# Kernel tuning notes

Measured on AMD Instinct MI355X. Metric: run time of the kernel, lower is better.

Reference implementation:

```python
import jax, jax.numpy as jnp
import numpy as np

B_SZ, L, N, H = 8, 4096, 256, 256
R_MIN, R_MAX, MAX_PHASE = 0.0, 1.0, 0.314


def setup_inputs() -> dict:
    key = jax.random.key(0)
    ks = jax.random.split(key, 8)
    x = jax.random.normal(ks[0], (B_SZ, L, H), jnp.float32)
    def glorot(k, shape):
        return jax.random.normal(k, shape, jnp.float32) * jnp.sqrt(2.0 / (shape[0] + shape[1])).astype(jnp.float32)
    B_re = glorot(ks[1], (N, H))
    B_im = glorot(ks[2], (N, H))
    C_re = glorot(ks[3], (H, N))
    C_im = glorot(ks[4], (H, N))
    # DiskRingRadius / DiskRingPhase initializers
    u1 = jax.random.uniform(ks[5], (N,), jnp.float32, 1e-6, 1.0)
    u2 = jax.random.uniform(ks[6], (N,), jnp.float32, 1e-6, 1.0)
    nu_log = jnp.log(-0.5 * jnp.log(u1 * (R_MAX ** 2 - R_MIN ** 2) + R_MIN ** 2))
    theta_log = jnp.log(MAX_PHASE * u2)
    D = jax.random.normal(ks[7], (H,), jnp.float32) * 0.05  # RandomNormal(stddev=0.05)
    return dict(x=x, B_re=B_re, B_im=B_im, C_re=C_re, C_im=C_im,
                nu_log=nu_log, theta_log=theta_log, D=D)


def reference(x, B_re, B_im, C_re, C_im, nu_log, theta_log, D):
    # Diagonal complex recurrence parameters
    Lambda = jnp.exp(jax.lax.complex(-jnp.exp(nu_log), jnp.exp(theta_log)))  # [N]
    gamma = jnp.sqrt(1.0 - jnp.abs(Lambda) ** 2).astype(jnp.complex64)       # [N]
    B_norm = (B_re + 1j * B_im).astype(jnp.complex64) * gamma[:, None]       # [N,H]
    C = (C_re + 1j * C_im).astype(jnp.complex64)                             # [H,N]

    # Input projection: [B,L,N] complex
    Bu = jnp.einsum('blh,nh->bln', x.astype(jnp.complex64), B_norm)
    Lambda_el = jnp.broadcast_to(Lambda, Bu.shape)

    def combine(a, b):
        la, ba = a
        lb, bb = b
        return (la * lb, lb * ba + bb)

    _, states = jax.lax.associative_scan(combine, (Lambda_el, Bu), axis=1)  # [B,L,N]

    y = jnp.real(jnp.einsum('bln,hn->blh', states, C))
    y = y + x * D  # H_in == H -> elementwise skip
    return y
```

## Files before the change

kernel.cpp:

```cpp
#include <hip/hip_runtime.h>
#include <hip/hip_bf16.h>
#include <math.h>

#define B_SZ 8
#define LSEQ 4096
#define NDIM 256
#define HDIM 256
#define MROWS (B_SZ * LSEQ)
#define CH 64
#define NC (LSEQ / CH)

#define BM 64
#define BN 128
#define BK 32
#define PAD 40
#define SSTR 68

typedef _Float16 half8 __attribute__((ext_vector_type(8)));
typedef _Float16 half4 __attribute__((ext_vector_type(4)));
typedef float fx4 __attribute__((ext_vector_type(4)));

__global__ void k_prep(const float* __restrict__ Bre, const float* __restrict__ Bim,
                       const float* __restrict__ Cre, const float* __restrict__ Cim,
                       const float* __restrict__ nu_log, const float* __restrict__ th_log,
                       _Float16* __restrict__ BreH, _Float16* __restrict__ BimH,
                       _Float16* __restrict__ CreH, _Float16* __restrict__ CimNH,
                       float* __restrict__ lamRe, float* __restrict__ lamIm,
                       float* __restrict__ powRe, float* __restrict__ powIm) {
    int r = blockIdx.x;
    int t = threadIdx.x;
    float nu  = expf(nu_log[r]);
    float th  = expf(th_log[r]);
    float mod = expf(-nu);
    float g   = sqrtf(fmaxf(1.0f - mod * mod, 0.0f));
    if (t == 0) {
        lamRe[r] = mod * cosf(th);
        lamIm[r] = mod * sinf(th);
    }
    int i = r * 256 + t;
    BreH[i]  = (_Float16)(Bre[i] * g);
    BimH[i]  = (_Float16)(Bim[i] * g);
    CreH[i]  = (_Float16)Cre[i];
    CimNH[i] = (_Float16)(-Cim[i]);
    if (r < CH) {
        float nuN = expf(nu_log[t]);
        float thN = expf(th_log[t]);
        float k   = (float)(r + 1);
        float mo  = expf(-nuN * k);
        powRe[r * 256 + t] = mo * cosf(thN * k);
        powIm[r * 256 + t] = mo * sinf(thN * k);
    }
}

__launch_bounds__(256)
__global__ void k_buscan(const float* __restrict__ x,
                         const _Float16* __restrict__ BreH,
                         const _Float16* __restrict__ BimH,
                         const float* __restrict__ lamRe,
                         const float* __restrict__ lamIm,
                         _Float16* __restrict__ stReH,
                         _Float16* __restrict__ stImH,
                         float* __restrict__ finRe,
                         float* __restrict__ finIm) {
    __shared__ __align__(16) _Float16 smem[25600];

    const int tid  = threadIdx.x;
    const int lane = tid & 63;
    const int wave = tid >> 6;
    const int wr   = wave >> 1;
    const int wc   = wave & 1;
    const int m0   = blockIdx.x * BM;
    const int n0   = blockIdx.y * BN;

    const int ar = tid >> 2, ac = (tid & 3) * 8;
    const int br = tid >> 1, bc = (tid & 1) * 16;

    const int fRC = lane & 15;
    const int fKg = (lane >> 4) * 8;

    fx4 accR[8], accI[8];
#pragma unroll
    for (int i = 0; i < 8; ++i) { accR[i] = (fx4)0.0f; accI[i] = (fx4)0.0f; }

    float4 xf0, xf1;
    half8 w0, w1, w2, w3;

    {
        const float* xp = x + (size_t)(m0 + ar) * HDIM + ac;
        xf0 = *(const float4*)xp;
        xf1 = *(const float4*)(xp + 4);
        const _Float16* bp1 = BreH + (size_t)(n0 + br) * HDIM + bc;
        const _Float16* bp2 = BimH + (size_t)(n0 + br) * HDIM + bc;
        w0 = *(const half8*)bp1;  w1 = *(const half8*)(bp1 + 8);
        w2 = *(const half8*)bp2;  w3 = *(const half8*)(bp2 + 8);
        half8 hv;
        hv[0]=(_Float16)xf0.x; hv[1]=(_Float16)xf0.y; hv[2]=(_Float16)xf0.z; hv[3]=(_Float16)xf0.w;
        hv[4]=(_Float16)xf1.x; hv[5]=(_Float16)xf1.y; hv[6]=(_Float16)xf1.z; hv[7]=(_Float16)xf1.w;
        *(half8*)&smem[ar * PAD + ac] = hv;
        *(half8*)&smem[2560 + br * PAD + bc] = w0;  *(half8*)&smem[2560 + br * PAD + bc + 8] = w1;
        *(half8*)&smem[7680 + br * PAD + bc] = w2;  *(half8*)&smem[7680 + br * PAD + bc + 8] = w3;
    }
    __syncthreads();

    int p = 0;
    for (int k0 = 0; k0 < HDIM; k0 += BK) {
        const int po = p * 12800;
        const bool nx = (k0 + BK) < HDIM;
        if (nx) {
            const float* xp = x + (size_t)(m0 + ar) * HDIM + k0 + BK + ac;
            xf0 = *(const float4*)xp;
            xf1 = *(const float4*)(xp + 4);
            const _Float16* bp1 = BreH + (size_t)(n0 + br) * HDIM + k0 + BK + bc;
            const _Float16* bp2 = BimH + (size_t)(n0 + br) * HDIM + k0 + BK + bc;
            w0 = *(const half8*)bp1;  w1 = *(const half8*)(bp1 + 8);
            w2 = *(const half8*)bp2;  w3 = *(const half8*)(bp2 + 8);
        }
        half8 af[2], bRf[4], bIf[4];
#pragma unroll
        for (int sm = 0; sm < 2; ++sm)
            af[sm] = *(const half8*)&smem[po + (wr * 32 + sm * 16 + fRC) * PAD + fKg];
#pragma unroll
        for (int sn = 0; sn < 4; ++sn) {
            bRf[sn] = *(const half8*)&smem[po + 2560 + (wc * 64 + sn * 16 + fRC) * PAD + fKg];
            bIf[sn] = *(const half8*)&smem[po + 7680 + (wc * 64 + sn * 16 + fRC) * PAD + fKg];
        }
#pragma unroll
        for (int sm = 0; sm < 2; ++sm)
#pragma unroll
            for (int sn = 0; sn < 4; ++sn) {
                accR[sm * 4 + sn] = __builtin_amdgcn_mfma_f32_16x16x32_f16(af[sm], bRf[sn], accR[sm * 4 + sn], 0, 0, 0);
                accI[sm * 4 + sn] = __builtin_amdgcn_mfma_f32_16x16x32_f16(af[sm], bIf[sn], accI[sm * 4 + sn], 0, 0, 0);
            }
        if (nx) {
            const int qo = (p ^ 1) * 12800;
            half8 hv;
            hv[0]=(_Float16)xf0.x; hv[1]=(_Float16)xf0.y; hv[2]=(_Float16)xf0.z; hv[3]=(_Float16)xf0.w;
            hv[4]=(_Float16)xf1.x; hv[5]=(_Float16)xf1.y; hv[6]=(_Float16)xf1.z; hv[7]=(_Float16)xf1.w;
            *(half8*)&smem[qo + ar * PAD + ac] = hv;
            *(half8*)&smem[qo + 2560 + br * PAD + bc] = w0;  *(half8*)&smem[qo + 2560 + br * PAD + bc + 8] = w1;
            *(half8*)&smem[qo + 7680 + br * PAD + bc] = w2;  *(half8*)&smem[qo + 7680 + br * PAD + bc + 8] = w3;
        }
        __syncthreads();
        p ^= 1;
    }

    _Float16* SRe = smem;
    _Float16* SIm = smem + 8704;

    const int rBase = (lane >> 4) * 4;
#pragma unroll
    for (int sm = 0; sm < 2; ++sm)
#pragma unroll
        for (int sn = 0; sn < 4; ++sn) {
            int col = wc * 64 + sn * 16 + fRC;
            int row = wr * 32 + sm * 16 + rBase;
            half4 h1, h2;
#pragma unroll
            for (int reg = 0; reg < 4; ++reg) {
                h1[reg] = (_Float16)accR[sm * 4 + sn][reg];
                h2[reg] = (_Float16)accI[sm * 4 + sn][reg];
            }
            *(half4*)&SRe[col * SSTR + row] = h1;
            *(half4*)&SIm[col * SSTR + row] = h2;
        }
    __syncthreads();

    if (tid < BN) {
        int col = tid;
        int n = n0 + col;
        float lr = lamRe[n], li = lamIm[n];
        _Float16* cR = &SRe[col * SSTR];
        _Float16* cI = &SIm[col * SSTR];
        float sr = 0.0f, si = 0.0f;
#pragma unroll 8
        for (int r = 0; r < CH; ++r) {
            float ur = (float)cR[r];
            float ui = (float)cI[r];
            float nr = fmaf(lr, sr, fmaf(-li, si, ur));
            float ni = fmaf(lr, si, fmaf(li, sr, ui));
            sr = nr; si = ni;
            cR[r] = (_Float16)sr;
            cI[r] = (_Float16)si;
        }
        int bb = blockIdx.x >> 6, cc = blockIdx.x & 63;
        size_t f = ((size_t)(bb * NC + cc)) * NDIM + n;
        finRe[f] = sr;
        finIm[f] = si;
    }
    __syncthreads();

    {
        int row = tid >> 2;
        int cb  = (tid & 3) * 32;
        size_t gbase = (size_t)(m0 + row) * NDIM + n0 + cb;
#pragma unroll
        for (int g = 0; g < 4; ++g) {
            half8 h1, h2;
#pragma unroll
            for (int e = 0; e < 8; ++e) {
                int col = cb + g * 8 + e;
                h1[e] = SRe[col * SSTR + row];
                h2[e] = SIm[col * SSTR + row];
            }
            *(half8*)(stReH + gbase + g * 8) = h1;
            *(half8*)(stImH + gbase + g * 8) = h2;
        }
    }
}

__launch_bounds__(256)
__global__ void k_carry(const float* __restrict__ lamRe,
                        const float* __restrict__ lamIm,
                        const float* __restrict__ finRe,
                        const float* __restrict__ finIm,
                        float* __restrict__ carRe,
                        float* __restrict__ carIm) {
    const int b = blockIdx.x;
    const int n = threadIdx.x;
    const float lr = lamRe[n];
    const float li = lamIm[n];
    float kr = 1.0f, ki = 0.0f;
#pragma unroll
    for (int i = 0; i < CH; ++i) {
        float t = kr * lr - ki * li;
        ki = fmaf(kr, li, ki * lr);
        kr = t;
    }
    float cr = 0.0f, ci = 0.0f;
#pragma unroll 8
    for (int c = 0; c < NC; ++c) {
        size_t idx = ((size_t)b * NC + c) * NDIM + n;
        carRe[idx] = cr;
        carIm[idx] = ci;
        float fr = finRe[idx];
        float fi = finIm[idx];
        float t = fmaf(kr, cr, fmaf(-ki, ci, fr));
        ci = fmaf(kr, ci, fmaf(ki, cr, fi));
        cr = t;
    }
}

__launch_bounds__(256)
__global__ void k_out(const _Float16* __restrict__ sReH,
                      const _Float16* __restrict__ sImH,
                      const _Float16* __restrict__ CreH,
                      const _Float16* __restrict__ CimNH,
                      const float* __restrict__ powRe,
                      const float* __restrict__ powIm,
                      const float* __restrict__ carRe,
                      const float* __restrict__ carIm,
                      const float* __restrict__ x,
                      const float* __restrict__ Dv,
                      float* __restrict__ y) {
    __shared__ __align__(16) _Float16 A1[2][BM * PAD];
    __shared__ __align__(16) _Float16 A2[2][BM * PAD];
    __shared__ __align__(16) _Float16 Cr[2][BN * PAD];
    __shared__ __align__(16) _Float16 Ci[2][BN * PAD];

    const int tid  = threadIdx.x;
    const int lane = tid & 63;
    const int wave = tid >> 6;
    const int wr   = wave >> 1;
    const int wc   = wave & 1;
    const int m0   = blockIdx.x * BM;
    const int h0   = blockIdx.y * BN;
    const int chunk = m0 >> 6;

    const int ar = tid >> 2, ac = (tid & 3) * 8;
    const int br = tid >> 1, bc = (tid & 1) * 16;

    const int fRC = lane & 15;
    const int fKg = (lane >> 4) * 8;

    fx4 acc[8];
#pragma unroll
    for (int i = 0; i < 8; ++i) acc[i] = (fx4)0.0f;

    half8 s1, s2, c0a, c0b, c1a, c1b;
    float4 pr0, pr1, pi0, pi1, cr0, cr1, ci0, ci1;

#define LOAD_STAGE(K0)                                                          \
    {                                                                           \
        size_t aOff = (size_t)(m0 + ar) * NDIM + (K0) + ac;                     \
        s1 = *(const half8*)(sReH + aOff);                                      \
        s2 = *(const half8*)(sImH + aOff);                                      \
        size_t pOff = (size_t)ar * NDIM + (K0) + ac;                            \
        pr0 = *(const float4*)(powRe + pOff); pr1 = *(const float4*)(powRe + pOff + 4); \
        pi0 = *(const float4*)(powIm + pOff); pi1 = *(const float4*)(powIm + pOff + 4); \
        size_t cOff = (size_t)chunk * NDIM + (K0) + ac;                         \
        cr0 = *(const float4*)(carRe + cOff); cr1 = *(const float4*)(carRe + cOff + 4); \
        ci0 = *(const float4*)(carIm + cOff); ci1 = *(const float4*)(carIm + cOff + 4); \
        const _Float16* cp1 = CreH  + (size_t)(h0 + br) * NDIM + (K0) + bc;     \
        const _Float16* cp2 = CimNH + (size_t)(h0 + br) * NDIM + (K0) + bc;     \
        c0a = *(const half8*)cp1;  c0b = *(const half8*)(cp1 + 8);              \
        c1a = *(const half8*)cp2;  c1b = *(const half8*)(cp2 + 8);              \
    }

#define WRITE_STAGE(P)                                                          \
    {                                                                           \
        float prA[8] = {pr0.x,pr0.y,pr0.z,pr0.w,pr1.x,pr1.y,pr1.z,pr1.w};       \
        float piA[8] = {pi0.x,pi0.y,pi0.z,pi0.w,pi1.x,pi1.y,pi1.z,pi1.w};       \
        float crA[8] = {cr0.x,cr0.y,cr0.z,cr0.w,cr1.x,cr1.y,cr1.z,cr1.w};       \
        float ciA[8] = {ci0.x,ci0.y,ci0.z,ci0.w,ci1.x,ci1.y,ci1.z,ci1.w};       \
        half8 h1, h2;                                                           \
        _Pragma("unroll")                                                       \
        for (int e = 0; e < 8; ++e) {                                           \
            float ur = fmaf(prA[e], crA[e], fmaf(-piA[e], ciA[e], (float)s1[e])); \
            float ui = fmaf(prA[e], ciA[e], fmaf( piA[e], crA[e], (float)s2[e])); \
            h1[e] = (_Float16)ur; h2[e] = (_Float16)ui;                         \
        }                                                                       \
        *(half8*)&A1[P][ar * PAD + ac] = h1;                                    \
        *(half8*)&A2[P][ar * PAD + ac] = h2;                                    \
        *(half8*)&Cr[P][br * PAD + bc] = c0a;  *(half8*)&Cr[P][br * PAD + bc + 8] = c0b; \
        *(half8*)&Ci[P][br * PAD + bc] = c1a;  *(half8*)&Ci[P][br * PAD + bc + 8] = c1b; \
    }

    LOAD_STAGE(0);
    WRITE_STAGE(0);
    __syncthreads();

    int p = 0;
    for (int k0 = 0; k0 < NDIM; k0 += BK) {
        const bool nx = (k0 + BK) < NDIM;
        if (nx) LOAD_STAGE(k0 + BK);
        half8 a1[2], a2[2], bRf[4], bIf[4];
#pragma unroll
        for (int sm = 0; sm < 2; ++sm) {
            a1[sm] = *(const half8*)&A1[p][(wr * 32 + sm * 16 + fRC) * PAD + fKg];
            a2[sm] = *(const half8*)&A2[p][(wr * 32 + sm * 16 + fRC) * PAD + fKg];
        }
#pragma unroll
        for (int sn = 0; sn < 4; ++sn) {
            bRf[sn] = *(const half8*)&Cr[p][(wc * 64 + sn * 16 + fRC) * PAD + fKg];
            bIf[sn] = *(const half8*)&Ci[p][(wc * 64 + sn * 16 + fRC) * PAD + fKg];
        }
#pragma unroll
        for (int sm = 0; sm < 2; ++sm)
#pragma unroll
            for (int sn = 0; sn < 4; ++sn) {
                acc[sm * 4 + sn] = __builtin_amdgcn_mfma_f32_16x16x32_f16(a1[sm], bRf[sn], acc[sm * 4 + sn], 0, 0, 0);
                acc[sm * 4 + sn] = __builtin_amdgcn_mfma_f32_16x16x32_f16(a2[sm], bIf[sn], acc[sm * 4 + sn], 0, 0, 0);
            }
        if (nx) WRITE_STAGE(p ^ 1);
        __syncthreads();
        p ^= 1;
    }

    float d[4];
#pragma unroll
    for (int sn = 0; sn < 4; ++sn) d[sn] = Dv[h0 + wc * 64 + sn * 16 + fRC];

    const int rBase = (lane >> 4) * 4;
#pragma unroll
    for (int sm = 0; sm < 2; ++sm)
#pragma unroll
        for (int sn = 0; sn < 4; ++sn) {
            int h = h0 + wc * 64 + sn * 16 + fRC;
#pragma unroll
            for (int reg = 0; reg < 4; ++reg) {
                int m = m0 + wr * 32 + sm * 16 + rBase + reg;
                size_t idx = (size_t)m * HDIM + h;
                y[idx] = fmaf(x[idx], d[sn], acc[sm * 4 + sn][reg]);
            }
        }
#undef LOAD_STAGE
#undef WRITE_STAGE
}

extern "C" void kernel_launch(void* const* d_in, const int* in_sizes, int n_in,
                              void* d_out, int out_size, void* d_ws, size_t ws_size,
                              hipStream_t stream) {
    const float* x      = (const float*)d_in[0];
    const float* B_re   = (const float*)d_in[1];
    const float* B_im   = (const float*)d_in[2];
    const float* C_re   = (const float*)d_in[3];
    const float* C_im   = (const float*)d_in[4];
    const float* nu_log = (const float*)d_in[5];
    const float* th_log = (const float*)d_in[6];
    const float* D      = (const float*)d_in[7];
    float* y = (float*)d_out;

    char* p = (char*)d_ws;
    _Float16* stReH = (_Float16*)p;  p += (size_t)MROWS * NDIM * 2;
    _Float16* stImH = (_Float16*)p;  p += (size_t)MROWS * NDIM * 2;
    _Float16* BreH  = (_Float16*)p;  p += (size_t)NDIM * HDIM * 2;
    _Float16* BimH  = (_Float16*)p;  p += (size_t)NDIM * HDIM * 2;
    _Float16* CreH  = (_Float16*)p;  p += (size_t)HDIM * NDIM * 2;
    _Float16* CimNH = (_Float16*)p;  p += (size_t)HDIM * NDIM * 2;
    float* lamRe = (float*)p;  p += NDIM * 4;
    float* lamIm = (float*)p;  p += NDIM * 4;
    float* powRe = (float*)p;  p += (size_t)CH * NDIM * 4;
    float* powIm = (float*)p;  p += (size_t)CH * NDIM * 4;
    float* finRe = (float*)p;  p += (size_t)B_SZ * NC * NDIM * 4;
    float* finIm = (float*)p;  p += (size_t)B_SZ * NC * NDIM * 4;
    float* carRe = (float*)p;  p += (size_t)B_SZ * NC * NDIM * 4;
    float* carIm = (float*)p;  p += (size_t)B_SZ * NC * NDIM * 4;

    k_prep<<<NDIM, 256, 0, stream>>>(B_re, B_im, C_re, C_im, nu_log, th_log,
                                     BreH, BimH, CreH, CimNH, lamRe, lamIm,
                                     powRe, powIm);

    dim3 gGemm(MROWS / BM, NDIM / BN);
    k_buscan<<<gGemm, 256, 0, stream>>>(x, BreH, BimH, lamRe, lamIm,
                                        stReH, stImH, finRe, finIm);

    k_carry<<<B_SZ, 256, 0, stream>>>(lamRe, lamIm, finRe, finIm, carRe, carIm);

    dim3 gOut(MROWS / BM, HDIM / BN);
    k_out<<<gOut, 256, 0, stream>>>(stReH, stImH, CreH, CimNH,
                                    powRe, powIm, carRe, carIm, x, D, y);
}
```

Measured before the change: 162.0 us.

## Swizzle LDS tiles, parallelize carry scan with wave shuffles, coalesce state stores

Replaces padded LDS tiles with an unpadded XOR-swizzled layout in both GEMM kernels, cutting LDS footprint and avoiding bank conflicts on fragment reads. The MFMA loops now load B fragments in two phases (real then imaginary) to lower register pressure. The cross-chunk carry kernel changes from a serial loop over 64 chunks per thread (8 blocks) to a per-wave Kogge-Stone complex scan using shuffles over 2048 waves. The state store pattern is reshuffled so that adjacent threads write adjacent 16-byte segments.

Result: faster. 150.9 us, median of 3 (-6.8%).

```diff
diff --git a/kernel.cpp b/kernel.cpp
--- a/kernel.cpp
+++ b/kernel.cpp
@@ -13,7 +13,6 @@
 #define BM 64
 #define BN 128
 #define BK 32
-#define PAD 40
 #define SSTR 68
 
 typedef _Float16 half8 __attribute__((ext_vector_type(8)));
@@ -62,7 +61,7 @@
                          _Float16* __restrict__ stImH,
                          float* __restrict__ finRe,
                          float* __restrict__ finIm) {
-    __shared__ __align__(16) _Float16 smem[25600];
+    __shared__ __align__(16) _Float16 smem[20480];
 
     const int tid  = threadIdx.x;
     const int lane = tid & 63;
@@ -73,10 +72,15 @@
     const int n0   = blockIdx.y * BN;
 
     const int ar = tid >> 2, ac = (tid & 3) * 8;
-    const int br = tid >> 1, bc = (tid & 1) * 16;
-
-    const int fRC = lane & 15;
-    const int fKg = (lane >> 4) * 8;
+    const int aw = ar * 32 + (((tid & 3) ^ ((tid >> 3) & 3)) * 8);
+
+    const int br = tid >> 1, g2 = tid & 1, bc = g2 * 16;
+    const int fb = (br >> 1) & 3;
+    const int bw0 = br * 32 + (((2 * g2)     ^ fb) * 8);
+    const int bw1 = br * 32 + (((2 * g2 + 1) ^ fb) * 8);
+
+    const int fRC   = lane & 15;
+    const int rslot = (((lane >> 4) ^ (fRC >> 1)) & 3) * 8;
 
     fx4 accR[8], accI[8];
 #pragma unroll
@@ -85,64 +89,64 @@
     float4 xf0, xf1;
     half8 w0, w1, w2, w3;
 
-    {
-        const float* xp = x + (size_t)(m0 + ar) * HDIM + ac;
-        xf0 = *(const float4*)xp;
-        xf1 = *(const float4*)(xp + 4);
-        const _Float16* bp1 = BreH + (size_t)(n0 + br) * HDIM + bc;
-        const _Float16* bp2 = BimH + (size_t)(n0 + br) * HDIM + bc;
-        w0 = *(const half8*)bp1;  w1 = *(const half8*)(bp1 + 8);
-        w2 = *(const half8*)bp2;  w3 = *(const half8*)(bp2 + 8);
-        half8 hv;
-        hv[0]=(_Float16)xf0.x; hv[1]=(_Float16)xf0.y; hv[2]=(_Float16)xf0.z; hv[3]=(_Float16)xf0.w;
-        hv[4]=(_Float16)xf1.x; hv[5]=(_Float16)xf1.y; hv[6]=(_Float16)xf1.z; hv[7]=(_Float16)xf1.w;
-        *(half8*)&smem[ar * PAD + ac] = hv;
-        *(half8*)&smem[2560 + br * PAD + bc] = w0;  *(half8*)&smem[2560 + br * PAD + bc + 8] = w1;
-        *(half8*)&smem[7680 + br * PAD + bc] = w2;  *(half8*)&smem[7680 + br * PAD + bc + 8] = w3;
-    }
+#define LOAD_T(K0)                                                          \
+    {                                                                       \
+        const float* xp = x + (size_t)(m0 + ar) * HDIM + (K0) + ac;         \
+        xf0 = *(const float4*)xp;                                           \
+        xf1 = *(const float4*)(xp + 4);                                     \
+        const _Float16* bp1 = BreH + (size_t)(n0 + br) * HDIM + (K0) + bc;  \
+        const _Float16* bp2 = BimH + (size_t)(n0 + br) * HDIM + (K0) + bc;  \
+        w0 = *(const half8*)bp1;  w1 = *(const half8*)(bp1 + 8);            \
+        w2 = *(const half8*)bp2;  w3 = *(const half8*)(bp2 + 8);            \
+    }
+#define WRITE_T(PO)                                                         \
+    {                                                                       \
+        half8 hv;                                                           \
+        hv[0]=(_Float16)xf0.x; hv[1]=(_Float16)xf0.y; hv[2]=(_Float16)xf0.z; hv[3]=(_Float16)xf0.w; \
+        hv[4]=(_Float16)xf1.x; hv[5]=(_Float16)xf1.y; hv[6]=(_Float16)xf1.z; hv[7]=(_Float16)xf1.w; \
+        *(half8*)&smem[(PO) + aw] = hv;                                     \
+        *(half8*)&smem[(PO) + 2048 + bw0] = w0;                             \
+        *(half8*)&smem[(PO) + 2048 + bw1] = w1;                             \
+        *(half8*)&smem[(PO) + 6144 + bw0] = w2;                             \
+        *(half8*)&smem[(PO) + 6144 + bw1] = w3;                             \
+    }
+
+    LOAD_T(0);
+    WRITE_T(0);
     __syncthreads();
 
     int p = 0;
     for (int k0 = 0; k0 < HDIM; k0 += BK) {
-        const int po = p * 12800;
+        const int po = p * 10240;
+        const int qo = (p ^ 1) * 10240;
         const bool nx = (k0 + BK) < HDIM;
-        if (nx) {
-            const float* xp = x + (size_t)(m0 + ar) * HDIM + k0 + BK + ac;
-            xf0 = *(const float4*)xp;
-            xf1 = *(const float4*)(xp + 4);
-            const _Float16* bp1 = BreH + (size_t)(n0 + br) * HDIM + k0 + BK + bc;
-            const _Float16* bp2 = BimH + (size_t)(n0 + br) * HDIM + k0 + BK + bc;
-            w0 = *(const half8*)bp1;  w1 = *(const half8*)(bp1 + 8);
-            w2 = *(const half8*)bp2;  w3 = *(const half8*)(bp2 + 8);
-        }
-        half8 af[2], bRf[4], bIf[4];
-#pragma unroll
-        for (int sm = 0; sm < 2; ++sm)
-            af[sm] = *(const half8*)&smem[po + (wr * 32 + sm * 16 + fRC) * PAD + fKg];
-#pragma unroll
-        for (int sn = 0; sn < 4; ++sn) {
-            bRf[sn] = *(const half8*)&smem[po + 2560 + (wc * 64 + sn * 16 + fRC) * PAD + fKg];
-            bIf[sn] = *(const half8*)&smem[po + 7680 + (wc * 64 + sn * 16 + fRC) * PAD + fKg];
-        }
-#pragma unroll
-        for (int sm = 0; sm < 2; ++sm)
-#pragma unroll
-            for (int sn = 0; sn < 4; ++sn) {
-                accR[sm * 4 + sn] = __builtin_amdgcn_mfma_f32_16x16x32_f16(af[sm], bRf[sn], accR[sm * 4 + sn], 0, 0, 0);
-                accI[sm * 4 + sn] = __builtin_amdgcn_mfma_f32_16x16x32_f16(af[sm], bIf[sn], accI[sm * 4 + sn], 0, 0, 0);
-            }
-        if (nx) {
-            const int qo = (p ^ 1) * 12800;
-            half8 hv;
-            hv[0]=(_Float16)xf0.x; hv[1]=(_Float16)xf0.y; hv[2]=(_Float16)xf0.z; hv[3]=(_Float16)xf0.w;
-            hv[4]=(_Float16)xf1.x; hv[5]=(_Float16)xf1.y; hv[6]=(_Float16)xf1.z; hv[7]=(_Float16)xf1.w;
-            *(half8*)&smem[qo + ar * PAD + ac] = hv;
-            *(half8*)&smem[qo + 2560 + br * PAD + bc] = w0;  *(half8*)&smem[qo + 2560 + br * PAD + bc + 8] = w1;
-            *(half8*)&smem[qo + 7680 + br * PAD + bc] = w2;  *(half8*)&smem[qo + 7680 + br * PAD + bc + 8] = w3;
-        }
+        if (nx) LOAD_T(k0 + BK);
+        half8 af[2], bf[4];
+#pragma unroll
+        for (int sm = 0; sm < 2; ++sm)
+            af[sm] = *(const half8*)&smem[po + (wr * 32 + sm * 16 + fRC) * 32 + rslot];
+#pragma unroll
+        for (int sn = 0; sn < 4; ++sn)
+            bf[sn] = *(const half8*)&smem[po + 2048 + (wc * 64 + sn * 16 + fRC) * 32 + rslot];
+#pragma unroll
+        for (int sm = 0; sm < 2; ++sm)
+#pragma unroll
+            for (int sn = 0; sn < 4; ++sn)
+                accR[sm * 4 + sn] = __builtin_amdgcn_mfma_f32_16x16x32_f16(af[sm], bf[sn], accR[sm * 4 + sn], 0, 0, 0);
+#pragma unroll
+        for (int sn = 0; sn < 4; ++sn)
+            bf[sn] = *(const half8*)&smem[po + 6144 + (wc * 64 + sn * 16 + fRC) * 32 + rslot];
+#pragma unroll
+        for (int sm = 0; sm < 2; ++sm)
+#pragma unroll
+            for (int sn = 0; sn < 4; ++sn)
+                accI[sm * 4 + sn] = __builtin_amdgcn_mfma_f32_16x16x32_f16(af[sm], bf[sn], accI[sm * 4 + sn], 0, 0, 0);
+        if (nx) WRITE_T(qo);
         __syncthreads();
         p ^= 1;
     }
+#undef LOAD_T
+#undef WRITE_T
 
     _Float16* SRe = smem;
     _Float16* SIm = smem + 8704;
@@ -191,19 +195,19 @@
 
     {
         int row = tid >> 2;
-        int cb  = (tid & 3) * 32;
+        int cb  = (tid & 3) * 8;
         size_t gbase = (size_t)(m0 + row) * NDIM + n0 + cb;
 #pragma unroll
         for (int g = 0; g < 4; ++g) {
             half8 h1, h2;
 #pragma unroll
             for (int e = 0; e < 8; ++e) {
-                int col = cb + g * 8 + e;
+                int col = cb + g * 32 + e;
                 h1[e] = SRe[col * SSTR + row];
                 h2[e] = SIm[col * SSTR + row];
             }
-            *(half8*)(stReH + gbase + g * 8) = h1;
-            *(half8*)(stImH + gbase + g * 8) = h2;
+            *(half8*)(stReH + gbase + g * 32) = h1;
+            *(half8*)(stImH + gbase + g * 32) = h2;
         }
     }
 }
@@ -215,29 +219,46 @@
                         const float* __restrict__ finIm,
                         float* __restrict__ carRe,
                         float* __restrict__ carIm) {
-    const int b = blockIdx.x;
-    const int n = threadIdx.x;
-    const float lr = lamRe[n];
-    const float li = lamIm[n];
-    float kr = 1.0f, ki = 0.0f;
-#pragma unroll
-    for (int i = 0; i < CH; ++i) {
-        float t = kr * lr - ki * li;
-        ki = fmaf(kr, li, ki * lr);
-        kr = t;
-    }
-    float cr = 0.0f, ci = 0.0f;
-#pragma unroll 8
-    for (int c = 0; c < NC; ++c) {
-        size_t idx = ((size_t)b * NC + c) * NDIM + n;
-        carRe[idx] = cr;
-        carIm[idx] = ci;
-        float fr = finRe[idx];
-        float fi = finIm[idx];
-        float t = fmaf(kr, cr, fmaf(-ki, ci, fr));
-        ci = fmaf(kr, ci, fmaf(ki, cr, fi));
-        cr = t;
-    }
+    const int tid  = threadIdx.x;
+    const int lane = tid & 63;
+    const int wv   = tid >> 6;
+    const int idx  = blockIdx.x * 4 + wv;
+    const int b    = idx >> 8;
+    const int n    = idx & 255;
+
+    float plr = lamRe[n], pli = lamIm[n];
+#pragma unroll
+    for (int i = 0; i < 6; ++i) {
+        float t = plr * plr - pli * pli;
+        pli = 2.0f * plr * pli;
+        plr = t;
+    }
+
+    size_t base = ((size_t)(b * NC + lane)) * NDIM + n;
+    float vr = finRe[base];
+    float vi = finIm[base];
+
+#pragma unroll
+    for (int d = 1; d < 64; d <<= 1) {
+        float vpr = __shfl_up(vr, d);
+        float vpi = __shfl_up(vi, d);
+        float lpr = __shfl_up(plr, d);
+        float lpi = __shfl_up(pli, d);
+        if (lane >= d) {
+            float nvr = fmaf(plr, vpr, fmaf(-pli, vpi, vr));
+            float nvi = fmaf(plr, vpi, fmaf(pli, vpr, vi));
+            vr = nvr; vi = nvi;
+            float t = plr * lpr - pli * lpi;
+            pli = fmaf(plr, lpi, pli * lpr);
+            plr = t;
+        }
+    }
+
+    float cr = __shfl_up(vr, 1);
+    float ci = __shfl_up(vi, 1);
+    if (lane == 0) { cr = 0.0f; ci = 0.0f; }
+    carRe[base] = cr;
+    carIm[base] = ci;
 }
 
 __launch_bounds__(256)
@@ -252,10 +273,10 @@
                       const float* __restrict__ x,
                       const float* __restrict__ Dv,
                       float* __restrict__ y) {
-    __shared__ __align__(16) _Float16 A1[2][BM * PAD];
-    __shared__ __align__(16) _Float16 A2[2][BM * PAD];
-    __shared__ __align__(16) _Float16 Cr[2][BN * PAD];
-    __shared__ __align__(16) _Float16 Ci[2][BN * PAD];
+    __shared__ __align__(16) _Float16 sA1[2][2048];
+    __shared__ __align__(16) _Float16 sA2[2][2048];
+    __shared__ __align__(16) _Float16 sCr[2][4096];
+    __shared__ __align__(16) _Float16 sCi[2][4096];
 
     const int tid  = threadIdx.x;
     const int lane = tid & 63;
@@ -267,10 +288,15 @@
     const int chunk = m0 >> 6;
 
     const int ar = tid >> 2, ac = (tid & 3) * 8;
-    const int br = tid >> 1, bc = (tid & 1) * 16;
-
-    const int fRC = lane & 15;
-    const int fKg = (lane >> 4) * 8;
+    const int aw = ar * 32 + (((tid & 3) ^ ((tid >> 3) & 3)) * 8);
+
+    const int br = tid >> 1, g2 = tid & 1, bc = g2 * 16;
+    const int fb = (br >> 1) & 3;
+    const int bw0 = br * 32 + (((2 * g2)     ^ fb) * 8);
+    const int bw1 = br * 32 + (((2 * g2 + 1) ^ fb) * 8);
+
+    const int fRC   = lane & 15;
+    const int rslot = (((lane >> 4) ^ (fRC >> 1)) & 3) * 8;
 
     fx4 acc[8];
 #pragma unroll
@@ -279,72 +305,78 @@
     half8 s1, s2, c0a, c0b, c1a, c1b;
     float4 pr0, pr1, pi0, pi1, cr0, cr1, ci0, ci1;
 
-#define LOAD_STAGE(K0)                                                          \
-    {                                                                           \
-        size_t aOff = (size_t)(m0 + ar) * NDIM + (K0) + ac;                     \
-        s1 = *(const half8*)(sReH + aOff);                                      \
-        s2 = *(const half8*)(sImH + aOff);                                      \
-        size_t pOff = (size_t)ar * NDIM + (K0) + ac;                            \
+#define LOAD_T(K0)                                                          \
+    {                                                                       \
+        size_t aOff = (size_t)(m0 + ar) * NDIM + (K0) + ac;                 \
+        s1 = *(const half8*)(sReH + aOff);                                  \
+        s2 = *(const half8*)(sImH + aOff);                                  \
+        size_t pOff = (size_t)ar * NDIM + (K0) + ac;                        \
         pr0 = *(const float4*)(powRe + pOff); pr1 = *(const float4*)(powRe + pOff + 4); \
         pi0 = *(const float4*)(powIm + pOff); pi1 = *(const float4*)(powIm + pOff + 4); \
-        size_t cOff = (size_t)chunk * NDIM + (K0) + ac;                         \
+        size_t cOff = (size_t)chunk * NDIM + (K0) + ac;                     \
         cr0 = *(const float4*)(carRe + cOff); cr1 = *(const float4*)(carRe + cOff + 4); \
         ci0 = *(const float4*)(carIm + cOff); ci1 = *(const float4*)(carIm + cOff + 4); \
-        const _Float16* cp1 = CreH  + (size_t)(h0 + br) * NDIM + (K0) + bc;     \
-        const _Float16* cp2 = CimNH + (size_t)(h0 + br) * NDIM + (K0) + bc;     \
-        c0a = *(const half8*)cp1;  c0b = *(const half8*)(cp1 + 8);              \
-        c1a = *(const half8*)cp2;  c1b = *(const half8*)(cp2 + 8);              \
-    }
-
-#define WRITE_STAGE(P)                                                          \
-    {                                                                           \
-        float prA[8] = {pr0.x,pr0.y,pr0.z,pr0.w,pr1.x,pr1.y,pr1.z,pr1.w};       \
-        float piA[8] = {pi0.x,pi0.y,pi0.z,pi0.w,pi1.x,pi1.y,pi1.z,pi1.w};       \
-        float crA[8] = {cr0.x,cr0.y,cr0.z,cr0.w,cr1.x,cr1.y,cr1.z,cr1.w};       \
-        float ciA[8] = {ci0.x,ci0.y,ci0.z,ci0.w,ci1.x,ci1.y,ci1.z,ci1.w};       \
-        half8 h1, h2;                                                           \
-        _Pragma("unroll")                                                       \
-        for (int e = 0; e < 8; ++e) {                                           \
+        const _Float16* cp1 = CreH  + (size_t)(h0 + br) * NDIM + (K0) + bc; \
+        const _Float16* cp2 = CimNH + (size_t)(h0 + br) * NDIM + (K0) + bc; \
+        c0a = *(const half8*)cp1;  c0b = *(const half8*)(cp1 + 8);          \
+        c1a = *(const half8*)cp2;  c1b = *(const half8*)(cp2 + 8);          \
+    }
+#define WRITE_T(PB)                                                         \
+    {                                                                       \
+        float prA[8] = {pr0.x,pr0.y,pr0.z,pr0.w,pr1.x,pr1.y,pr1.z,pr1.w};   \
+        float piA[8] = {pi0.x,pi0.y,pi0.z,pi0.w,pi1.x,pi1.y,pi1.z,pi1.w};   \
+        float crA[8] = {cr0.x,cr0.y,cr0.z,cr0.w,cr1.x,cr1.y,cr1.z,cr1.w};   \
+        float ciA[8] = {ci0.x,ci0.y,ci0.z,ci0.w,ci1.x,ci1.y,ci1.z,ci1.w};   \
+        half8 h1, h2;                                                       \
+        _Pragma("unroll")                                                   \
+        for (int e = 0; e < 8; ++e) {                                       \
             float ur = fmaf(prA[e], crA[e], fmaf(-piA[e], ciA[e], (float)s1[e])); \
             float ui = fmaf(prA[e], ciA[e], fmaf( piA[e], crA[e], (float)s2[e])); \
-            h1[e] = (_Float16)ur; h2[e] = (_Float16)ui;                         \
-        }                                                                       \
-        *(half8*)&A1[P][ar * PAD + ac] = h1;                                    \
-        *(half8*)&A2[P][ar * PAD + ac] = h2;                                    \
-        *(half8*)&Cr[P][br * PAD + bc] = c0a;  *(half8*)&Cr[P][br * PAD + bc + 8] = c0b; \
-        *(half8*)&Ci[P][br * PAD + bc] = c1a;  *(half8*)&Ci[P][br * PAD + bc + 8] = c1b; \
-    }
-
-    LOAD_STAGE(0);
-    WRITE_STAGE(0);
+            h1[e] = (_Float16)ur; h2[e] = (_Float16)ui;                     \
+        }                                                                   \
+        *(half8*)&sA1[PB][aw] = h1;                                         \
+        *(half8*)&sA2[PB][aw] = h2;                                         \
+        *(half8*)&sCr[PB][bw0] = c0a;  *(half8*)&sCr[PB][bw1] = c0b;        \
+        *(half8*)&sCi[PB][bw0] = c1a;  *(half8*)&sCi[PB][bw1] = c1b;        \
+    }
+
+    LOAD_T(0);
+    WRITE_T(0);
     __syncthreads();
 
     int p = 0;
     for (int k0 = 0; k0 < NDIM; k0 += BK) {
         const bool nx = (k0 + BK) < NDIM;
-        if (nx) LOAD_STAGE(k0 + BK);
-        half8 a1[2], a2[2], bRf[4], bIf[4];
-#pragma unroll
-        for (int sm = 0; sm < 2; ++sm) {
-            a1[sm] = *(const half8*)&A1[p][(wr * 32 + sm * 16 + fRC) * PAD + fKg];
-            a2[sm] = *(const half8*)&A2[p][(wr * 32 + sm * 16 + fRC) * PAD + fKg];
-        }
-#pragma unroll
-        for (int sn = 0; sn < 4; ++sn) {
-            bRf[sn] = *(const half8*)&Cr[p][(wc * 64 + sn * 16 + fRC) * PAD + fKg];
-            bIf[sn] = *(const half8*)&Ci[p][(wc * 64 + sn * 16 + fRC) * PAD + fKg];
-        }
-#pragma unroll
-        for (int sm = 0; sm < 2; ++sm)
-#pragma unroll
-            for (int sn = 0; sn < 4; ++sn) {
-                acc[sm * 4 + sn] = __builtin_amdgcn_mfma_f32_16x16x32_f16(a1[sm], bRf[sn], acc[sm * 4 + sn], 0, 0, 0);
-                acc[sm * 4 + sn] = __builtin_amdgcn_mfma_f32_16x16x32_f16(a2[sm], bIf[sn], acc[sm * 4 + sn], 0, 0, 0);
-            }
-        if (nx) WRITE_STAGE(p ^ 1);
+        if (nx) LOAD_T(k0 + BK);
+        half8 af[2], bf[4];
+#pragma unroll
+        for (int sm = 0; sm < 2; ++sm)
+            af[sm] = *(const half8*)&sA1[p][(wr * 32 + sm * 16 + fRC) * 32 + rslot];
+#pragma unroll
+        for (int sn = 0; sn < 4; ++sn)
+            bf[sn] = *(const half8*)&sCr[p][(wc * 64 + sn * 16 + fRC) * 32 + rslot];
+#pragma unroll
+        for (int sm = 0; sm < 2; ++sm)
+#pragma unroll
+            for (int sn = 0; sn < 4; ++sn)
+                acc[sm * 4 + sn] = __builtin_amdgcn_mfma_f32_16x16x32_f16(af[sm], bf[sn], acc[sm * 4 + sn], 0, 0, 0);
+#pragma unroll
+        for (int sm = 0; sm < 2; ++sm)
+            af[sm] = *(const half8*)&sA2[p][(wr * 32 + sm * 16 + fRC) * 32 + rslot];
+#pragma unroll
+        for (int sn = 0; sn < 4; ++sn)
+            bf[sn] = *(const half8*)&sCi[p][(wc * 64 + sn * 16 + fRC) * 32 + rslot];
+#pragma unroll
+        for (int sm = 0; sm < 2; ++sm)
+#pragma unroll
+            for (int sn = 0; sn < 4; ++sn)
+                acc[sm * 4 + sn] = __builtin_amdgcn_mfma_f32_16x16x32_f16(af[sm], bf[sn], acc[sm * 4 + sn], 0, 0, 0);
+        if (nx) WRITE_T(p ^ 1);
         __syncthreads();
         p ^= 1;
     }
+#undef LOAD_T
+#undef WRITE_T
 
     float d[4];
 #pragma unroll
@@ -363,8 +395,6 @@
                 y[idx] = fmaf(x[idx], d[sn], acc[sm * 4 + sn][reg]);
             }
         }
-#undef LOAD_STAGE
-#undef WRITE_STAGE
 }
 
 extern "C" void kernel_launch(void* const* d_in, const int* in_sizes, int n_in,
@@ -404,7 +434,8 @@
     k_buscan<<<gGemm, 256, 0, stream>>>(x, BreH, BimH, lamRe, lamIm,
                                         stReH, stImH, finRe, finIm);
 
-    k_carry<<<B_SZ, 256, 0, stream>>>(lamRe, lamIm, finRe, finIm, carRe, carIm);
+    k_carry<<<(B_SZ * NDIM) / 4, 256, 0, stream>>>(lamRe, lamIm, finRe, finIm,
+                                                   carRe, carIm);
 
     dim3 gOut(MROWS / BM, HDIM / BN);
     k_out<<<gOut, 256, 0, stream>>>(stReH, stImH, CreH, CimNH,
```
